# Kernel tuning notes

Measured on AMD Instinct MI355X. Metric: run time of the kernel, lower is better.

Reference implementation:

```python
import jax, jax.numpy as jnp
import numpy as np

N_NODES = 50000
E_DIM = 128
H_DIM = 256
OUT_DIM = 2
N_EDGES = 800000
NEG_SLOPE = 0.01  # nn.LeakyReLU default


def gcn_conv(x, W, b, src, dst, n):
    """PyG GCNConv: h = x @ W; add self-loops; sym-normalized scatter-add; + bias."""
    h = x @ W  # [N, H]
    loop = jnp.arange(n, dtype=src.dtype)
    s = jnp.concatenate([src, loop])
    d = jnp.concatenate([dst, loop])
    w = jnp.ones_like(s, dtype=h.dtype)
    deg = jax.ops.segment_sum(w, d, num_segments=n)  # in-degree incl. self-loop
    dis = jnp.where(deg > 0, jax.lax.rsqrt(deg), jnp.zeros_like(deg))
    norm = dis[s] * dis[d]  # [E+N]
    msg = h[s] * norm[:, None]  # gather + scale
    out = jax.ops.segment_sum(msg, d, num_segments=n)  # scatter-add to targets
    return out + b


def setup_inputs() -> dict:
    key = jax.random.key(0)
    ks = jax.random.split(key, 12)
    inp = {
        "mask_feature": jax.random.normal(ks[0], (N_NODES, E_DIM), jnp.float32),
        "feature": jax.random.normal(ks[1], (N_NODES, E_DIM), jnp.float32),
        "edge_index": jax.random.randint(ks[2], (2, N_EDGES), 0, N_NODES, jnp.int64 if jax.config.jax_enable_x64 else jnp.int32),
        "edge_type": jax.random.randint(ks[3], (N_EDGES,), 0, 2, jnp.int64 if jax.config.jax_enable_x64 else jnp.int32),
        # learned parameters
        "W_in": jax.random.normal(ks[4], (E_DIM, H_DIM), jnp.float32) * 0.05,
        "b_in": jnp.zeros((H_DIM,), jnp.float32),
        "Wg1": jax.random.normal(ks[5], (H_DIM, H_DIM), jnp.float32) * 0.05,
        "bg1": jnp.zeros((H_DIM,), jnp.float32),
        "Wg2": jax.random.normal(ks[6], (H_DIM, H_DIM), jnp.float32) * 0.05,
        "bg2": jnp.zeros((H_DIM,), jnp.float32),
        "W_out": jax.random.normal(ks[7], (H_DIM, OUT_DIM), jnp.float32) * 0.05,
        "b_out": jnp.zeros((OUT_DIM,), jnp.float32),
    }
    return inp


def reference(mask_feature, feature, edge_index, edge_type,
              W_in, b_in, Wg1, bg1, Wg2, bg2, W_out, b_out):
    src, dst = edge_index[0], edge_index[1]
    n = mask_feature.shape[0]
    # main branch
    x = jax.nn.leaky_relu(mask_feature @ W_in + b_in, NEG_SLOPE)
    x = gcn_conv(x, Wg1, bg1, src, dst, n)
    # dropout is identity at inference
    x = gcn_conv(x, Wg2, bg2, src, dst, n)
    x = x @ W_out + b_out  # [N, out_dim]
    # mask branch
    m = jax.nn.leaky_relu((feature - mask_feature) @ W_in + b_in, NEG_SLOPE)
    m = m @ W_out + b_out  # [N, out_dim]
    return x * m
```

## Files before the change

### kernel.cpp

```cpp
#include <hip/hip_runtime.h>


#define NEG_SLOPE 0.01f
constexpr int HD = 256;
constexpr int CHUNK = 4096;
constexpr int BSTRIDE = 8192;

typedef __bf16 bf16x8 __attribute__((ext_vector_type(8)));
typedef unsigned short u16x8 __attribute__((ext_vector_type(8)));
typedef float f32x4 __attribute__((ext_vector_type(4)));

#define MFMA16 __builtin_amdgcn_mfma_f32_16x16x32_bf16

__device__ inline void split1(float v, unsigned short& h, unsigned short& l) {
  unsigned u = __float_as_uint(v);
  unsigned hb = u & 0xFFFF0000u;
  float lf = v - __uint_as_float(hb);
  unsigned ul = __float_as_uint(lf);
  h = (unsigned short)(hb >> 16);
  l = (unsigned short)((ul + 0x7FFFu + ((ul >> 16) & 1u)) >> 16);
}

__global__ __launch_bounds__(256) void k_prep(
    const float* __restrict__ Win, u16x8* __restrict__ Wf,
    const float* __restrict__ Wg1, const float* __restrict__ Wg2,
    const float* __restrict__ Wo, const float* __restrict__ bg1,
    const float* __restrict__ bg2, const float* __restrict__ bo,
    float* __restrict__ wb, float* __restrict__ uv, int* __restrict__ cur) {
  __shared__ float wt[256][2];
  const int bid = blockIdx.x, tid = threadIdx.x;
  if (bid < 32) {
    int f = bid * 4 + (tid >> 6);
    int lane = tid & 63;
    int nt = f >> 3, ks = (f >> 1) & 3, hl = f & 1;
    int n = nt * 16 + (lane & 15);
    int k0 = ks * 32 + (lane >> 4) * 8;
    u16x8 outv;
    #pragma unroll
    for (int j = 0; j < 8; ++j) {
      unsigned short h, l;
      split1(Win[(size_t)(k0 + j) * HD + n], h, l);
      outv[j] = hl ? l : h;
    }
    Wf[f * 64 + lane] = outv;
  } else if (bid == 32) {
    int r = tid;
    float s0 = 0.f, s1 = 0.f;
    for (int k = 0; k < 256; ++k) {
      float w = Wg2[r * 256 + k];
      s0 = fmaf(w, Wo[k * 2 + 0], s0);
      s1 = fmaf(w, Wo[k * 2 + 1], s1);
    }
    wt[r][0] = s0; wt[r][1] = s1;
    __syncthreads();
    float b0 = 0.f, b1 = 0.f;
    for (int k = 0; k < 256; ++k) {
      float w = Wg1[r * 256 + k];
      b0 = fmaf(w, wt[k][0], b0);
      b1 = fmaf(w, wt[k][1], b1);
    }
    wb[r * 2 + 0] = b0; wb[r * 2 + 1] = b1;
    if (r < 2) {
      float u = 0.f, v = 0.f;
      for (int k = 0; k < 256; ++k) {
        u = fmaf(bg1[k], wt[k][r], u);
        v = fmaf(bg2[k], Wo[k * 2 + r], v);
      }
      uv[r] = u;
      uv[2 + r] = v + bo[r];
    }
  } else {
    cur[tid] = 0;
  }
}

__global__ __launch_bounds__(256) void k_scatter(
    const int* __restrict__ src, const int* __restrict__ dst,
    int* __restrict__ cur, unsigned* __restrict__ packed, int E) {
  __shared__ int bins[256];
  __shared__ int lcur[256];
  const int t = threadIdx.x, b = blockIdx.x;
  bins[t] = 0;
  __syncthreads();
  const int e0 = b * CHUNK, e1 = min(e0 + CHUNK, E);
  for (int e = e0 + t; e < e1; e += 256)
    atomicAdd(&bins[dst[e] >> 8], 1);
  __syncthreads();
  lcur[t] = atomicAdd(&cur[t], bins[t]);
  __syncthreads();
  for (int e = e0 + t; e < e1; e += 256) {
    int d = dst[e], s = src[e];
    int bin = d >> 8;
    int pos = atomicAdd(&lcur[bin], 1);
    packed[(size_t)bin * BSTRIDE + pos] = ((unsigned)d << 16) | (unsigned)s;
  }
}

__device__ __forceinline__ void gemm_both32(
    const float* __restrict__ mf, const float* __restrict__ fe,
    const u16x8* __restrict__ Wf, const float* __restrict__ bi,
    const float* __restrict__ wb, const float* __restrict__ Wo,
    const float* __restrict__ bo, float4* __restrict__ q,
    float* __restrict__ Pm, int M, int gbid) {
  const int tid = threadIdx.x;
  const int lane = tid & 63, wid = tid >> 6;
  const int base = gbid * 128 + wid * 32;
  const int kb = (lane >> 4) * 8;

  bf16x8 ahi[2][4], alo[2][4], mhi[2][4], mlo[2][4];
  #pragma unroll
  for (int h = 0; h < 2; ++h) {
    int arow = base + h * 16 + (lane & 15);
    if (arow >= M) arow = M - 1;
    const float* ap = mf + (size_t)arow * 128 + kb;
    const float* fp = fe + (size_t)arow * 128 + kb;
    #pragma unroll
    for (int ks = 0; ks < 4; ++ks) {
      float x[8], y[8];
      *(float4*)&x[0] = *(const float4*)(ap + ks * 32);
      *(float4*)&x[4] = *(const float4*)(ap + ks * 32 + 4);
      *(float4*)&y[0] = *(const float4*)(fp + ks * 32);
      *(float4*)&y[4] = *(const float4*)(fp + ks * 32 + 4);
      u16x8 hA, lA, hM, lM;
      #pragma unroll
      for (int j = 0; j < 8; ++j) {
        unsigned short hh, ll;
        split1(x[j], hh, ll);        hA[j] = hh; lA[j] = ll;
        split1(y[j] - x[j], hh, ll); hM[j] = hh; lM[j] = ll;
      }
      ahi[h][ks] = __builtin_bit_cast(bf16x8, hA);
      alo[h][ks] = __builtin_bit_cast(bf16x8, lA);
      mhi[h][ks] = __builtin_bit_cast(bf16x8, hM);
      mlo[h][ks] = __builtin_bit_cast(bf16x8, lM);
    }
  }

  const u16x8* wp = Wf + lane;
  float s0[2][4] = {}, s1[2][4] = {}, t0[2][4] = {}, t1[2][4] = {};

  u16x8 bA[8], bB[8];
  #pragma unroll
  for (int f = 0; f < 8; ++f) bA[f] = wp[f * 64];

  auto COMPUTE = [&](const u16x8* b, int nt) {
    f32x4 aM[2] = {{0,0,0,0},{0,0,0,0}}, aK[2] = {{0,0,0,0},{0,0,0,0}};
    #pragma unroll
    for (int ks = 0; ks < 4; ++ks) {
      bf16x8 bh = __builtin_bit_cast(bf16x8, b[ks * 2 + 0]);
      bf16x8 bl = __builtin_bit_cast(bf16x8, b[ks * 2 + 1]);
      #pragma unroll
      for (int h = 0; h < 2; ++h) {
        aM[h] = MFMA16(ahi[h][ks], bh, aM[h], 0, 0, 0);
        aM[h] = MFMA16(alo[h][ks], bh, aM[h], 0, 0, 0);
        aM[h] = MFMA16(ahi[h][ks], bl, aM[h], 0, 0, 0);
        aK[h] = MFMA16(mhi[h][ks], bh, aK[h], 0, 0, 0);
        aK[h] = MFMA16(mlo[h][ks], bh, aK[h], 0, 0, 0);
        aK[h] = MFMA16(mhi[h][ks], bl, aK[h], 0, 0, 0);
      }
    }
    const int col = nt * 16 + (lane & 15);
    const float bc = bi[col];
    const float w0 = wb[col * 2 + 0], w1 = wb[col * 2 + 1];
    const float v0 = Wo[col * 2 + 0], v1 = Wo[col * 2 + 1];
    #pragma unroll
    for (int h = 0; h < 2; ++h) {
      #pragma unroll
      for (int r = 0; r < 4; ++r) {
        float a = aM[h][r] + bc; a = a > 0.f ? a : NEG_SLOPE * a;
        s0[h][r] = fmaf(a, w0, s0[h][r]); s1[h][r] = fmaf(a, w1, s1[h][r]);
        float m = aK[h][r] + bc; m = m > 0.f ? m : NEG_SLOPE * m;
        t0[h][r] = fmaf(m, v0, t0[h][r]); t1[h][r] = fmaf(m, v1, t1[h][r]);
      }
    }
  };

  #pragma unroll 1
  for (int nt = 0; nt < 16; nt += 2) {
    #pragma unroll
    for (int f = 0; f < 8; ++f) bB[f] = wp[((nt + 1) * 8 + f) * 64];
    COMPUTE(bA, nt);
    if (nt + 2 < 16) {
      #pragma unroll
      for (int f = 0; f < 8; ++f) bA[f] = wp[((nt + 2) * 8 + f) * 64];
    }
    COMPUTE(bB, nt + 1);
  }

  #pragma unroll
  for (int o = 1; o < 16; o <<= 1) {
    #pragma unroll
    for (int h = 0; h < 2; ++h) {
      #pragma unroll
      for (int r = 0; r < 4; ++r) {
        s0[h][r] += __shfl_xor(s0[h][r], o, 16);
        s1[h][r] += __shfl_xor(s1[h][r], o, 16);
        t0[h][r] += __shfl_xor(t0[h][r], o, 16);
        t1[h][r] += __shfl_xor(t1[h][r], o, 16);
      }
    }
  }
  if ((lane & 15) == 0) {
    float bo0 = bo[0], bo1 = bo[1];
    #pragma unroll
    for (int h = 0; h < 2; ++h) {
      #pragma unroll
      for (int r = 0; r < 4; ++r) {
        int row = base + h * 16 + (lane >> 4) * 4 + r;
        if (row < M) {
          float* qf = (float*)&q[row];
          qf[1] = s0[h][r];
          qf[2] = s1[h][r];
          Pm[row * 2 + 0] = t0[h][r] + bo0;
          Pm[row * 2 + 1] = t1[h][r] + bo1;
        }
      }
    }
  }
}

__global__ __launch_bounds__(256) void k_main(
    const float* __restrict__ mf, const float* __restrict__ fe,
    const u16x8* __restrict__ Wf, const float* __restrict__ bi,
    const float* __restrict__ wb, const float* __restrict__ Wo,
    const float* __restrict__ bo, float4* __restrict__ q, float* __restrict__ Pm,
    const unsigned* __restrict__ packed, const int* __restrict__ cur,
    int* __restrict__ rp, int* __restrict__ csr, int N, int Gg) {
  if ((int)blockIdx.x < Gg) {
    gemm_both32(mf, fe, Wf, bi, wb, Wo, bo, q, Pm, N, blockIdx.x);
    return;
  }
  __shared__ int cnt[256];
  __shared__ int sc[256];
  __shared__ int wsum[4];
  const int t = threadIdx.x;
  const int B = blockIdx.x - Gg;
  const int lane = t & 63, wid = t >> 6;
  int tot = cur[t], incl = tot;
  #pragma unroll
  for (int o = 1; o < 64; o <<= 1) {
    int tmp = __shfl_up(incl, o, 64);
    if (lane >= o) incl += tmp;
  }
  if (lane == 63) wsum[wid] = incl;
  __syncthreads();
  int woff = 0;
  for (int w = 0; w < wid; ++w) woff += wsum[w];
  sc[t] = woff + incl - tot;
  __syncthreads();
  const int base = sc[B];
  const int ecnt = cur[B];
  const unsigned* pk = packed + (size_t)B * BSTRIDE;
  cnt[t] = 0;
  __syncthreads();
  for (int i = t; i < ecnt; i += 256)
    atomicAdd(&cnt[(pk[i] >> 16) & 0xFF], 1);
  __syncthreads();
  int v = cnt[t];
  incl = v;
  #pragma unroll
  for (int o = 1; o < 64; o <<= 1) {
    int tmp = __shfl_up(incl, o, 64);
    if (lane >= o) incl += tmp;
  }
  if (lane == 63) wsum[wid] = incl;
  __syncthreads();
  woff = 0;
  for (int w = 0; w < wid; ++w) woff += wsum[w];
  const int off = woff + incl - v;
  const int node = B * 256 + t;
  if (node < N) {
    rp[node] = base + off;
    ((float*)&q[node])[0] = rsqrtf((float)(v + 1));
  } else if (node == N) {
    rp[N] = base + off;
  }
  __syncthreads();
  cnt[t] = off;
  __syncthreads();
  for (int i = t; i < ecnt; i += 256) {
    unsigned pv = pk[i];
    int pos = base + atomicAdd(&cnt[(pv >> 16) & 0xFF], 1);
    csr[pos] = (int)(pv & 0xFFFFu);
  }
}

__global__ __launch_bounds__(256) void k_gather1(
    const int* __restrict__ rp, const int* __restrict__ csr,
    const float4* __restrict__ q, const float* __restrict__ uv,
    float* __restrict__ T2, int N) {
  int t = threadIdx.x;
  int n = blockIdx.x * 64 + (t >> 2);
  int l = t & 3;
  if (n >= N) return;
  int s0 = rp[n], s1 = rp[n + 1];
  float a0 = 0.f, a1 = 0.f;
  int j = s0 + l;
  for (; j + 4 < s1; j += 8) {
    int sa = csr[j], sb = csr[j + 4];
    float4 qa = q[sa], qb = q[sb];
    a0 = fmaf(qa.x, qa.y, a0); a1 = fmaf(qa.x, qa.z, a1);
    a0 = fmaf(qb.x, qb.y, a0); a1 = fmaf(qb.x, qb.z, a1);
  }
  if (j < s1) {
    float4 qa = q[csr[j]];
    a0 = fmaf(qa.x, qa.y, a0); a1 = fmaf(qa.x, qa.z, a1);
  }
  a0 += __shfl_xor(a0, 1, 4); a1 += __shfl_xor(a1, 1, 4);
  a0 += __shfl_xor(a0, 2, 4); a1 += __shfl_xor(a1, 2, 4);
  if (l == 0) {
    float4 qn = q[n];
    float d = qn.x;
    T2[n * 2 + 0] = d * (d * fmaf(d, qn.y, a0) + uv[0]);
    T2[n * 2 + 1] = d * (d * fmaf(d, qn.z, a1) + uv[1]);
  }
}

__global__ __launch_bounds__(256) void k_gather2(
    const int* __restrict__ rp, const int* __restrict__ csr,
    const float* __restrict__ T2, const float4* __restrict__ q,
    const float* __restrict__ uv, const float* __restrict__ Pm,
    float* __restrict__ out, int N) {
  int t = threadIdx.x;
  int n = blockIdx.x * 64 + (t >> 2);
  int l = t & 3;
  if (n >= N) return;
  int s0 = rp[n], s1 = rp[n + 1];
  float a0 = 0.f, a1 = 0.f;
  int j = s0 + l;
  for (; j + 4 < s1; j += 8) {
    int sa = csr[j], sb = csr[j + 4];
    float2 va = *(const float2*)&T2[sa * 2];
    float2 vb = *(const float2*)&T2[sb * 2];
    a0 += va.x + vb.x; a1 += va.y + vb.y;
  }
  if (j < s1) {
    float2 va = *(const float2*)&T2[csr[j] * 2];
    a0 += va.x; a1 += va.y;
  }
  a0 += __shfl_xor(a0, 1, 4); a1 += __shfl_xor(a1, 1, 4);
  a0 += __shfl_xor(a0, 2, 4); a1 += __shfl_xor(a1, 2, 4);
  if (l == 0) {
    float d = q[n].x;
    float2 tv = *(const float2*)&T2[n * 2];
    float z0 = d * (tv.x + a0) + uv[2];
    float z1 = d * (tv.y + a1) + uv[3];
    out[n * 2 + 0] = z0 * Pm[n * 2 + 0];
    out[n * 2 + 1] = z1 * Pm[n * 2 + 1];
  }
}

extern "C" void kernel_launch(void* const* d_in, const int* in_sizes, int n_in,
                              void* d_out, int out_size, void* d_ws, size_t ws_size,
                              hipStream_t stream) {
  const float* mf  = (const float*)d_in[0];
  const float* fe  = (const float*)d_in[1];
  const int*   ei  = (const int*)d_in[2];
  const float* Win = (const float*)d_in[4];
  const float* bin = (const float*)d_in[5];
  const float* Wg1 = (const float*)d_in[6];
  const float* bg1 = (const float*)d_in[7];
  const float* Wg2 = (const float*)d_in[8];
  const float* bg2 = (const float*)d_in[9];
  const float* Wo  = (const float*)d_in[10];
  const float* bo  = (const float*)d_in[11];
  float* out = (float*)d_out;

  const int ED = 128;
  const int N = in_sizes[0] / ED;
  const int E = in_sizes[3];
  const int* src = ei;
  const int* dst = ei + E;

  char* ws = (char*)d_ws;
  size_t off = 0;
  auto carve = [&](size_t bytes) {
    char* p = ws + off;
    off += (bytes + 255) & ~(size_t)255;
    return p;
  };
  int*      cur    = (int*)carve(256 * 4);
  unsigned* packed = (unsigned*)carve((size_t)256 * BSTRIDE * 4);
  int*      csr    = (int*)carve((size_t)E * 4);
  int*      rp     = (int*)carve((size_t)(N + 1) * 4);
  float4*   q      = (float4*)carve((size_t)N * 16);
  float*    T2     = (float*)carve((size_t)N * 2 * 4);
  float*    Pm     = (float*)carve((size_t)N * 2 * 4);
  float*    wb     = (float*)carve((size_t)HD * 2 * 4);
  float*    uv     = (float*)carve(4 * 4);
  u16x8*    Wf     = (u16x8*)carve((size_t)128 * 64 * 16);
  (void)ws_size; (void)n_in; (void)out_size;

  const int NB  = (E + CHUNK - 1) / CHUNK;
  const int NP2 = (N + 255) / 256;
  const int Gg  = (N + 127) / 128;
  const int Gt  = (N + 63) / 64;

  k_prep<<<34, 256, 0, stream>>>(Win, Wf, Wg1, Wg2, Wo, bg1, bg2, bo, wb, uv, cur);
  k_scatter<<<NB, 256, 0, stream>>>(src, dst, cur, packed, E);
  k_main<<<Gg + NP2, 256, 0, stream>>>(mf, fe, Wf, bin, wb, Wo, bo, q, Pm,
                                       packed, cur, rp, csr, N, Gg);
  k_gather1<<<Gt, 256, 0, stream>>>(rp, csr, q, uv, T2, N);
  k_gather2<<<Gt, 256, 0, stream>>>(rp, csr, T2, q, uv, Pm, out, N);
}
```

Measured before the change: 100.7 us.

## Stage scatter and CSR writes through LDS, split GEMM into LDS-weight kernel

k_scatter now sorts each chunk's packed edges into LDS by bin and then writes them to global memory as contiguous runs, so scattered single-word writes become coalesced ones. The CSR build moves into its own kernel that also sorts into LDS before writing csr contiguously. The GEMM becomes a separate 512-thread kernel that stages the full split-bf16 W_in (128 KB) in shared memory instead of streaming it per wave from global. The cost is that the CSR build and the GEMM no longer share one launch and cannot overlap, and the large LDS footprint per block may cut occupancy.

```diff
diff --git a/kernel.cpp b/kernel.cpp
--- a/kernel.cpp
+++ b/kernel.cpp
@@ -77,34 +77,120 @@
 __global__ __launch_bounds__(256) void k_scatter(
     const int* __restrict__ src, const int* __restrict__ dst,
     int* __restrict__ cur, unsigned* __restrict__ packed, int E) {
-  __shared__ int bins[256];
-  __shared__ int lcur[256];
+  __shared__ int bins[256], lstart[256], gbase[256], lcur[256];
+  __shared__ int wsum[4];
+  __shared__ unsigned sbuf[CHUNK];
   const int t = threadIdx.x, b = blockIdx.x;
+  const int lane = t & 63, wid = t >> 6;
   bins[t] = 0;
   __syncthreads();
-  const int e0 = b * CHUNK, e1 = min(e0 + CHUNK, E);
+  const int e0 = b * CHUNK, e1 = min(e0 + CHUNK, E), m = e1 - e0;
   for (int e = e0 + t; e < e1; e += 256)
     atomicAdd(&bins[dst[e] >> 8], 1);
   __syncthreads();
-  lcur[t] = atomicAdd(&cur[t], bins[t]);
+  {
+    int v = bins[t], incl = v;
+    #pragma unroll
+    for (int o = 1; o < 64; o <<= 1) {
+      int tmp = __shfl_up(incl, o, 64);
+      if (lane >= o) incl += tmp;
+    }
+    if (lane == 63) wsum[wid] = incl;
+    __syncthreads();
+    int woff = 0;
+    for (int w = 0; w < wid; ++w) woff += wsum[w];
+    int st = woff + incl - v;
+    lstart[t] = st;
+    lcur[t] = st;
+    gbase[t] = v ? atomicAdd(&cur[t], v) : 0;
+  }
   __syncthreads();
   for (int e = e0 + t; e < e1; e += 256) {
     int d = dst[e], s = src[e];
-    int bin = d >> 8;
-    int pos = atomicAdd(&lcur[bin], 1);
-    packed[(size_t)bin * BSTRIDE + pos] = ((unsigned)d << 16) | (unsigned)s;
-  }
-}
-
-__device__ __forceinline__ void gemm_both32(
+    int slot = atomicAdd(&lcur[d >> 8], 1);
+    sbuf[slot] = ((unsigned)d << 16) | (unsigned)s;
+  }
+  __syncthreads();
+  for (int i = t; i < m; i += 256) {
+    unsigned pv = sbuf[i];
+    int bin = pv >> 24;
+    packed[(size_t)bin * BSTRIDE + gbase[bin] + (i - lstart[bin])] = pv;
+  }
+}
+
+__global__ __launch_bounds__(256) void k_p2(
+    const unsigned* __restrict__ packed, const int* __restrict__ cur,
+    int* __restrict__ rp, float4* __restrict__ q, int* __restrict__ csr, int N) {
+  __shared__ int cnt[256], sc[256];
+  __shared__ int wsum[4];
+  __shared__ unsigned short sbuf[BSTRIDE];
+  const int t = threadIdx.x;
+  const int B = blockIdx.x;
+  const int lane = t & 63, wid = t >> 6;
+  int tot = cur[t], incl = tot;
+  #pragma unroll
+  for (int o = 1; o < 64; o <<= 1) {
+    int tmp = __shfl_up(incl, o, 64);
+    if (lane >= o) incl += tmp;
+  }
+  if (lane == 63) wsum[wid] = incl;
+  __syncthreads();
+  int woff = 0;
+  for (int w = 0; w < wid; ++w) woff += wsum[w];
+  sc[t] = woff + incl - tot;
+  __syncthreads();
+  const int base = sc[B];
+  const int ecnt = cur[B];
+  const unsigned* pk = packed + (size_t)B * BSTRIDE;
+  cnt[t] = 0;
+  __syncthreads();
+  for (int i = t; i < ecnt; i += 256)
+    atomicAdd(&cnt[(pk[i] >> 16) & 0xFF], 1);
+  __syncthreads();
+  int v = cnt[t];
+  incl = v;
+  #pragma unroll
+  for (int o = 1; o < 64; o <<= 1) {
+    int tmp = __shfl_up(incl, o, 64);
+    if (lane >= o) incl += tmp;
+  }
+  if (lane == 63) wsum[wid] = incl;
+  __syncthreads();
+  woff = 0;
+  for (int w = 0; w < wid; ++w) woff += wsum[w];
+  const int off = woff + incl - v;
+  const int node = B * 256 + t;
+  if (node < N) {
+    rp[node] = base + off;
+    ((float*)&q[node])[0] = rsqrtf((float)(v + 1));
+  } else if (node == N) {
+    rp[N] = base + off;
+  }
+  __syncthreads();
+  cnt[t] = off;
+  __syncthreads();
+  for (int i = t; i < ecnt; i += 256) {
+    unsigned pv = pk[i];
+    int slot = atomicAdd(&cnt[(pv >> 16) & 0xFF], 1);
+    sbuf[slot] = (unsigned short)(pv & 0xFFFFu);
+  }
+  __syncthreads();
+  for (int i = t; i < ecnt; i += 256)
+    csr[base + i] = (int)sbuf[i];
+}
+
+__global__ __launch_bounds__(512, 2) void k_gemm(
     const float* __restrict__ mf, const float* __restrict__ fe,
     const u16x8* __restrict__ Wf, const float* __restrict__ bi,
     const float* __restrict__ wb, const float* __restrict__ Wo,
     const float* __restrict__ bo, float4* __restrict__ q,
-    float* __restrict__ Pm, int M, int gbid) {
+    float* __restrict__ Pm, int M) {
+  __shared__ u16x8 sWf[8192];
   const int tid = threadIdx.x;
+  #pragma unroll
+  for (int i = 0; i < 16; ++i) sWf[tid + i * 512] = Wf[tid + i * 512];
   const int lane = tid & 63, wid = tid >> 6;
-  const int base = gbid * 128 + wid * 32;
+  const int base = blockIdx.x * 256 + wid * 32;
   const int kb = (lane >> 4) * 8;
 
   bf16x8 ahi[2][4], alo[2][4], mhi[2][4], mlo[2][4];
@@ -134,20 +220,16 @@
       mlo[h][ks] = __builtin_bit_cast(bf16x8, lM);
     }
   }
-
-  const u16x8* wp = Wf + lane;
+  __syncthreads();
+
   float s0[2][4] = {}, s1[2][4] = {}, t0[2][4] = {}, t1[2][4] = {};
-
-  u16x8 bA[8], bB[8];
-  #pragma unroll
-  for (int f = 0; f < 8; ++f) bA[f] = wp[f * 64];
-
-  auto COMPUTE = [&](const u16x8* b, int nt) {
+  #pragma unroll 1
+  for (int nt = 0; nt < 16; ++nt) {
     f32x4 aM[2] = {{0,0,0,0},{0,0,0,0}}, aK[2] = {{0,0,0,0},{0,0,0,0}};
     #pragma unroll
     for (int ks = 0; ks < 4; ++ks) {
-      bf16x8 bh = __builtin_bit_cast(bf16x8, b[ks * 2 + 0]);
-      bf16x8 bl = __builtin_bit_cast(bf16x8, b[ks * 2 + 1]);
+      bf16x8 bh = __builtin_bit_cast(bf16x8, sWf[(nt * 8 + ks * 2 + 0) * 64 + lane]);
+      bf16x8 bl = __builtin_bit_cast(bf16x8, sWf[(nt * 8 + ks * 2 + 1) * 64 + lane]);
       #pragma unroll
       for (int h = 0; h < 2; ++h) {
         aM[h] = MFMA16(ahi[h][ks], bh, aM[h], 0, 0, 0);
@@ -172,18 +254,6 @@
         t0[h][r] = fmaf(m, v0, t0[h][r]); t1[h][r] = fmaf(m, v1, t1[h][r]);
       }
     }
-  };
-
-  #pragma unroll 1
-  for (int nt = 0; nt < 16; nt += 2) {
-    #pragma unroll
-    for (int f = 0; f < 8; ++f) bB[f] = wp[((nt + 1) * 8 + f) * 64];
-    COMPUTE(bA, nt);
-    if (nt + 2 < 16) {
-      #pragma unroll
-      for (int f = 0; f < 8; ++f) bA[f] = wp[((nt + 2) * 8 + f) * 64];
-    }
-    COMPUTE(bB, nt + 1);
   }
 
   #pragma unroll
@@ -215,72 +285,6 @@
         }
       }
     }
-  }
-}
-
-__global__ __launch_bounds__(256) void k_main(
-    const float* __restrict__ mf, const float* __restrict__ fe,
-    const u16x8* __restrict__ Wf, const float* __restrict__ bi,
-    const float* __restrict__ wb, const float* __restrict__ Wo,
-    const float* __restrict__ bo, float4* __restrict__ q, float* __restrict__ Pm,
-    const unsigned* __restrict__ packed, const int* __restrict__ cur,
-    int* __restrict__ rp, int* __restrict__ csr, int N, int Gg) {
-  if ((int)blockIdx.x < Gg) {
-    gemm_both32(mf, fe, Wf, bi, wb, Wo, bo, q, Pm, N, blockIdx.x);
-    return;
-  }
-  __shared__ int cnt[256];
-  __shared__ int sc[256];
-  __shared__ int wsum[4];
-  const int t = threadIdx.x;
-  const int B = blockIdx.x - Gg;
-  const int lane = t & 63, wid = t >> 6;
-  int tot = cur[t], incl = tot;
-  #pragma unroll
-  for (int o = 1; o < 64; o <<= 1) {
-    int tmp = __shfl_up(incl, o, 64);
-    if (lane >= o) incl += tmp;
-  }
-  if (lane == 63) wsum[wid] = incl;
-  __syncthreads();
-  int woff = 0;
-  for (int w = 0; w < wid; ++w) woff += wsum[w];
-  sc[t] = woff + incl - tot;
-  __syncthreads();
-  const int base = sc[B];
-  const int ecnt = cur[B];
-  const unsigned* pk = packed + (size_t)B * BSTRIDE;
-  cnt[t] = 0;
-  __syncthreads();
-  for (int i = t; i < ecnt; i += 256)
-    atomicAdd(&cnt[(pk[i] >> 16) & 0xFF], 1);
-  __syncthreads();
-  int v = cnt[t];
-  incl = v;
-  #pragma unroll
-  for (int o = 1; o < 64; o <<= 1) {
-    int tmp = __shfl_up(incl, o, 64);
-    if (lane >= o) incl += tmp;
-  }
-  if (lane == 63) wsum[wid] = incl;
-  __syncthreads();
-  woff = 0;
-  for (int w = 0; w < wid; ++w) woff += wsum[w];
-  const int off = woff + incl - v;
-  const int node = B * 256 + t;
-  if (node < N) {
-    rp[node] = base + off;
-    ((float*)&q[node])[0] = rsqrtf((float)(v + 1));
-  } else if (node == N) {
-    rp[N] = base + off;
-  }
-  __syncthreads();
-  cnt[t] = off;
-  __syncthreads();
-  for (int i = t; i < ecnt; i += 256) {
-    unsigned pv = pk[i];
-    int pos = base + atomicAdd(&cnt[(pv >> 16) & 0xFF], 1);
-    csr[pos] = (int)(pv & 0xFFFFu);
   }
 }
 
@@ -392,13 +396,13 @@
 
   const int NB  = (E + CHUNK - 1) / CHUNK;
   const int NP2 = (N + 255) / 256;
-  const int Gg  = (N + 127) / 128;
+  const int Gg  = (N + 255) / 256;
   const int Gt  = (N + 63) / 64;
 
   k_prep<<<34, 256, 0, stream>>>(Win, Wf, Wg1, Wg2, Wo, bg1, bg2, bo, wb, uv, cur);
   k_scatter<<<NB, 256, 0, stream>>>(src, dst, cur, packed, E);
-  k_main<<<Gg + NP2, 256, 0, stream>>>(mf, fe, Wf, bin, wb, Wo, bo, q, Pm,
-                                       packed, cur, rp, csr, N, Gg);
+  k_p2<<<NP2, 256, 0, stream>>>(packed, cur, rp, q, csr, N);
+  k_gemm<<<Gg, 512, 0, stream>>>(mf, fe, Wf, bin, wb, Wo, bo, q, Pm, N);
   k_gather1<<<Gt, 256, 0, stream>>>(rp, csr, q, uv, T2, N);
   k_gather2<<<Gt, 256, 0, stream>>>(rp, csr, T2, q, uv, Pm, out, N);
 }
```

Result: no change. 100.8 us (+0.1%).
